# Kernel tuning notes

Measured on AMD Instinct MI355X. Metric: run time of the kernel, lower is better.

Reference implementation:

```python
import jax, jax.numpy as jnp
import numpy as np

K_DIM = 128

def setup_inputs() -> dict:
    key = jax.random.key(0)
    k1, k2, k3, k4 = jax.random.split(key, 4)
    B, S, D = 4, 4096, 1024
    input_vec = jax.random.normal(k1, (B, S, D), dtype=jnp.float32)
    # 'normal' Keras initializer ~ RandomNormal(stddev=0.05)
    weight_query = jax.random.normal(k2, (D, K_DIM), dtype=jnp.float32) * 0.05
    weight_key = jax.random.normal(k3, (D, K_DIM), dtype=jnp.float32) * 0.05
    weight_value = jax.random.normal(k4, (D, K_DIM), dtype=jnp.float32) * 0.05
    return {"input_vec": input_vec, "weight_query": weight_query,
            "weight_key": weight_key, "weight_value": weight_value}

def reference(input_vec, weight_query, weight_key, weight_value):
    # Q/K/V projections: [B,S,D] @ [D,K] -> [B,S,K]
    q = jnp.einsum('bsd,dk->bsk', input_vec, weight_query)
    k = jnp.einsum('bsd,dk->bsk', input_vec, weight_key)
    v = jnp.einsum('bsd,dk->bsk', input_vec, weight_value)
    scale = 1.0 / jnp.sqrt(jnp.asarray(K_DIM, dtype=q.dtype))
    # full score matrix [B,S,S], softmax over last axis (keys)
    scores = jnp.einsum('bqk,bsk->bqs', q, k) * scale
    attn = jax.nn.softmax(scores, axis=-1)
    return jnp.einsum('bqs,bsk->bqk', attn, v)
```

## Files before the change

### kernel.cpp

```cpp
#include <hip/hip_runtime.h>
#include <hip/hip_bf16.h>
#include <math.h>

#define B_  4
#define S_  4096
#define D_  1024
#define KD_ 128
#define NSPL 4
#define NIT64 (S_ / NSPL / 64)

typedef __attribute__((ext_vector_type(8))) short short8;
typedef __attribute__((ext_vector_type(4))) float f32x4;
typedef __attribute__((ext_vector_type(16))) float f32x16;
typedef __attribute__((ext_vector_type(4))) unsigned short us4;
typedef __attribute__((ext_vector_type(4))) unsigned int u32x4;

__device__ __forceinline__ unsigned short f2bf(float f) {
    __hip_bfloat16 h = __float2bfloat16(f);
    return *reinterpret_cast<unsigned short*>(&h);
}

__device__ __forceinline__ f32x4 mfma_bf16(short8 a, short8 b, f32x4 c) {
    return __builtin_amdgcn_mfma_f32_16x16x32_bf16(a, b, c, 0, 0, 0);
}

__device__ __forceinline__ f32x16 mfma32_bf16(short8 a, short8 b, f32x16 c) {
    return __builtin_amdgcn_mfma_f32_32x32x16_bf16(a, b, c, 0, 0, 0);
}

__device__ __forceinline__ unsigned int cvt_pk_bf16(float lo, float hi_) {
    unsigned int r;
    asm("v_cvt_pk_bf16_f32 %0, %1, %2" : "=v"(r) : "v"(lo), "v"(hi_));
    return r;
}

__device__ __forceinline__ void g2l16(const void* g, void* l) {
    __builtin_amdgcn_global_load_lds(
        (const __attribute__((address_space(1))) unsigned int*)g,
        (__attribute__((address_space(3))) unsigned int*)l, 16, 0, 0);
}

__global__ void convert_w_kernel(const float* __restrict__ wq,
                                 const float* __restrict__ wk,
                                 const float* __restrict__ wv,
                                 unsigned short* __restrict__ wt) {
    int t = blockIdx.x * 256 + threadIdx.x;
    int w = t >> 14;
    int r = t & 16383;
    int n = r & 127;
    int k8 = r >> 7;
    const float* src = (w == 0) ? wq : (w == 1) ? wk : wv;
    float scale = (w == 0) ? 0.12751725551033443f : 1.0f;
    short8 v;
#pragma unroll
    for (int i = 0; i < 8; ++i)
        v[i] = (short)f2bf(src[(size_t)(k8 * 8 + i) * KD_ + n] * scale);
    *reinterpret_cast<short8*>(&wt[(size_t)w * KD_ * D_ + (size_t)n * D_ + k8 * 8]) = v;
}

__global__ __launch_bounds__(512) void proj_kernel(
        const float* __restrict__ X, const unsigned short* __restrict__ Wt,
        unsigned short* __restrict__ Qo, unsigned short* __restrict__ Ko,
        unsigned short* __restrict__ Vt) {
    const int bid = blockIdx.x;
    const int g = bid / 24;
    const int local = bid - g * 24;
    const int which = local >> 3;
    const int mtile = g * 8 + (local & 7);
    const int m0 = mtile * 128;
    const int tid = threadIdx.x;
    const int lane = tid & 63;
    const int wid = tid >> 6;
    const int wr = wid >> 2, wc = wid & 3;
    const int l15 = lane & 15, l4 = lane >> 4;

    __shared__ __align__(16) unsigned short Asm[128 * 64];
    __shared__ __align__(16) unsigned short Bsm[128 * 64];
    __shared__ __align__(16) unsigned short Tsm[128 * 128];

    const unsigned short* W = Wt + (size_t)which * KD_ * D_;

    f32x4 acc[4][2];
#pragma unroll
    for (int r = 0; r < 4; ++r)
#pragma unroll
        for (int c = 0; c < 2; ++c) acc[r][c] = (f32x4)0.0f;

    for (int k0 = 0; k0 < D_; k0 += 64) {
#pragma unroll
        for (int i = 0; i < 4; ++i) {
            int f = tid + i * 512;
            int row = f >> 4, c4 = f & 15;
            float4 xv = *reinterpret_cast<const float4*>(
                &X[(size_t)(m0 + row) * D_ + k0 + c4 * 4]);
            us4 h;
            h.x = f2bf(xv.x); h.y = f2bf(xv.y); h.z = f2bf(xv.z); h.w = f2bf(xv.w);
            int gw = c4 >> 1, half = c4 & 1;
            *reinterpret_cast<us4*>(
                &Asm[row * 64 + ((gw ^ (row & 7)) * 8) + half * 4]) = h;
        }
#pragma unroll
        for (int i = 0; i < 2; ++i) {
            int gg = tid + i * 512;
            int n = gg >> 3, c8 = gg & 7;
            *reinterpret_cast<short8*>(&Bsm[n * 64 + ((c8 ^ (n & 7)) * 8)]) =
                *reinterpret_cast<const short8*>(&W[(size_t)n * D_ + k0 + c8 * 8]);
        }
        __syncthreads();

        short8 a[4][2], b[2][2];
#pragma unroll
        for (int rt = 0; rt < 4; ++rt)
#pragma unroll
            for (int kc = 0; kc < 2; ++kc) {
                int row = wr * 64 + rt * 16 + l15;
                int gr = kc * 4 + l4;
                a[rt][kc] = *reinterpret_cast<const short8*>(
                    &Asm[row * 64 + ((gr ^ (row & 7)) * 8)]);
            }
#pragma unroll
        for (int ct = 0; ct < 2; ++ct)
#pragma unroll
            for (int kc = 0; kc < 2; ++kc) {
                int row = wc * 32 + ct * 16 + l15;
                int gr = kc * 4 + l4;
                b[ct][kc] = *reinterpret_cast<const short8*>(
                    &Bsm[row * 64 + ((gr ^ (row & 7)) * 8)]);
            }
        __builtin_amdgcn_s_setprio(1);
#pragma unroll
        for (int kc = 0; kc < 2; ++kc)
#pragma unroll
            for (int rt = 0; rt < 4; ++rt)
#pragma unroll
                for (int ct = 0; ct < 2; ++ct)
                    acc[rt][ct] = mfma_bf16(a[rt][kc], b[ct][kc], acc[rt][ct]);
        __builtin_amdgcn_s_setprio(0);
        __syncthreads();
    }

    if (which < 2) {
        unsigned short* O = (which == 0) ? Qo : Ko;
#pragma unroll
        for (int rt = 0; rt < 4; ++rt)
#pragma unroll
            for (int ct = 0; ct < 2; ++ct)
#pragma unroll
                for (int j = 0; j < 4; ++j) {
                    int row = m0 + wr * 64 + rt * 16 + l4 * 4 + j;
                    int col = wc * 32 + ct * 16 + l15;
                    O[(size_t)row * KD_ + col] = f2bf(acc[rt][ct][j]);
                }
    } else {
#pragma unroll
        for (int rt = 0; rt < 4; ++rt)
#pragma unroll
            for (int ct = 0; ct < 2; ++ct)
#pragma unroll
                for (int j = 0; j < 4; ++j) {
                    int row = wr * 64 + rt * 16 + l4 * 4 + j;
                    int col = wc * 32 + ct * 16 + l15;
                    Tsm[col * 128 + row] = f2bf(acc[rt][ct][j]);
                }
        __syncthreads();
        int bb = m0 >> 12;
        int s0 = m0 & 4095;
#pragma unroll
        for (int i = 0; i < 4; ++i) {
            int gg = tid + i * 512;
            int n = gg >> 4, s8 = gg & 15;
            *reinterpret_cast<short8*>(
                &Vt[(size_t)bb * KD_ * S_ + (size_t)n * S_ + s0 + s8 * 8]) =
                *reinterpret_cast<short8*>(&Tsm[n * 128 + s8 * 8]);
        }
    }
}

__global__ __launch_bounds__(256, 2) void attn_split_kernel(
        const unsigned short* __restrict__ Q,
        const unsigned short* __restrict__ Kb,
        const unsigned short* __restrict__ Vt,
        unsigned short* __restrict__ part16, float* __restrict__ lsumP) {
    const int bid = blockIdx.x;
    const int b  = bid & 3;
    const int s  = (bid >> 2) & 3;
    const int qt = bid >> 4;
    const int tid = threadIdx.x;
    const int lane = tid & 63;
    const int wid = tid >> 6;
    const int q0 = qt * 128;
    const int l31 = lane & 31;
    const int hi  = lane >> 5;

    __shared__ __align__(16) unsigned short Ksm[2][64 * 128];
    __shared__ __align__(16) unsigned short Vsm[2][128 * 64];

    short8 aq[8];
    {
        const unsigned short* qrow =
            Q + ((size_t)(b * S_ + q0 + wid * 32 + l31)) * KD_;
#pragma unroll
        for (int kc = 0; kc < 8; ++kc)
            aq[kc] = *reinterpret_cast<const short8*>(&qrow[kc * 16 + hi * 8]);
    }

    f32x16 o[4];
#pragma unroll
    for (int dt = 0; dt < 4; ++dt) o[dt] = (f32x16)0.0f;
    float lsA = 0.0f, lsB = 0.0f;

    const unsigned short* Kbase = Kb + (size_t)b * S_ * KD_;
    const unsigned short* Vbase = Vt + (size_t)b * KD_ * S_;

    auto STAGE = [&](int buf, int kt) {
#pragma unroll
        for (int i = 0; i < 4; ++i) {
            int d = i * 256 + wid * 64 + lane;
            int row = d >> 4, c = d & 15;
            g2l16(&Kbase[(size_t)(kt * 64 + row) * KD_ + ((c ^ (row & 15)) * 8)],
                  &Ksm[buf][(i * 256 + wid * 64) * 8]);
        }
#pragma unroll
        for (int i = 0; i < 4; ++i) {
            int d = i * 256 + wid * 64 + lane;
            int row = d >> 3, c = d & 7;
            g2l16(&Vbase[(size_t)row * S_ + kt * 64 + ((c ^ (row & 7)) * 8)],
                  &Vsm[buf][(i * 256 + wid * 64) * 8]);
        }
    };

    const int base = s * NIT64;
    STAGE(0, base);

    for (int it = 0; it < NIT64; ++it) {
        asm volatile("s_waitcnt vmcnt(0)" ::: "memory");
        __builtin_amdgcn_s_barrier();
        if (it + 1 < NIT64) STAGE((it + 1) & 1, base + it + 1);

        const unsigned short* ksm = &Ksm[it & 1][0];
        const unsigned short* vsm = &Vsm[it & 1][0];

#pragma unroll
        for (int h = 0; h < 2; ++h) {
            f32x16 sf = (f32x16)0.0f;
            __builtin_amdgcn_s_setprio(1);
#pragma unroll
            for (int kc = 0; kc < 8; ++kc) {
                int row = h * 32 + l31;
                short8 bk = *reinterpret_cast<const short8*>(
                    &ksm[row * 128 + (((kc * 2 + hi) ^ (l31 & 15)) * 8)]);
                sf = mfma32_bf16(bk, aq[kc], sf);
            }
            __builtin_amdgcn_s_setprio(0);

            float p[16];
#pragma unroll
            for (int r = 0; r < 16; ++r) {
                p[r] = exp2f(sf[r]);
                if (r & 1) lsB += p[r]; else lsA += p[r];
            }

            short8 pa[2];
#pragma unroll
            for (int c = 0; c < 2; ++c) {
                u32x4 wv;
#pragma unroll
                for (int e = 0; e < 2; ++e) {
                    unsigned int X = cvt_pk_bf16(p[8 * c + 2 * e], p[8 * c + 2 * e + 1]);
                    unsigned int Y = cvt_pk_bf16(p[8 * c + 4 + 2 * e], p[8 * c + 4 + 2 * e + 1]);
                    unsigned int Ss = hi ? X : Y;
                    unsigned int T = __shfl_xor(Ss, 32);
                    wv[e]     = hi ? T : X;
                    wv[2 + e] = hi ? Y : T;
                }
                pa[c] = __builtin_bit_cast(short8, wv);
            }

            __builtin_amdgcn_s_setprio(1);
#pragma unroll
            for (int c = 0; c < 2; ++c)
#pragma unroll
                for (int dt = 0; dt < 4; ++dt) {
                    int row = dt * 32 + l31;
                    int gr = (h * 2 + c) * 2 + hi;
                    short8 bv = *reinterpret_cast<const short8*>(
                        &vsm[row * 64 + ((gr ^ (row & 7)) * 8)]);
                    o[dt] = mfma32_bf16(pa[c], bv, o[dt]);
                }
            __builtin_amdgcn_s_setprio(0);
        }
    }

    float lsum = lsA + lsB;
    lsum += __shfl_xor(lsum, 32);

    const int tile = (qt << 2) | b;
    unsigned short* Po = part16 + ((size_t)tile * NSPL + s) * 16384;
#pragma unroll
    for (int r = 0; r < 16; ++r) {
        int row = wid * 32 + (r & 3) + 8 * (r >> 2) + 4 * hi;
#pragma unroll
        for (int dt = 0; dt < 4; ++dt)
            Po[row * 128 + dt * 32 + l31] = f2bf(o[dt][r]);
    }
    if (hi == 0)
        lsumP[((size_t)tile * NSPL + s) * 128 + wid * 32 + l31] = lsum;
}

__global__ __launch_bounds__(256) void merge_kernel(
        const unsigned short* __restrict__ part16,
        const float* __restrict__ lsumP, float* __restrict__ Out) {
    const int th = blockIdx.x;
    const int tile = th >> 1;
    const int half = th & 1;
    const int b = tile & 3, qt = tile >> 2;
    const int r0 = half * 64;
    const int tid = threadIdx.x;
    __shared__ float inv[64];
    if (tid < 64) {
        const float* lp = lsumP + (size_t)tile * (NSPL * 128) + r0;
        float t = 0.0f;
#pragma unroll
        for (int s = 0; s < NSPL; ++s) t += lp[s * 128 + tid];
        inv[tid] = 1.0f / t;
    }
    __syncthreads();
    const unsigned short* p = part16 + (size_t)tile * NSPL * 16384 + r0 * 128;
    float* Ob = Out + ((size_t)b * S_ + qt * 128 + r0) * KD_;
#pragma unroll
    for (int i = 0; i < 4; ++i) {
        int g = tid + i * 256;
        int row = g >> 4;
        float acc8[8] = {0, 0, 0, 0, 0, 0, 0, 0};
#pragma unroll
        for (int s = 0; s < NSPL; ++s) {
            short8 v = *reinterpret_cast<const short8*>(&p[s * 16384 + g * 8]);
#pragma unroll
            for (int j = 0; j < 8; ++j) {
                unsigned int u = ((unsigned int)(unsigned short)v[j]) << 16;
                acc8[j] += __uint_as_float(u);
            }
        }
        float iv = inv[row];
        float4 r0v, r1v;
        r0v.x = acc8[0] * iv; r0v.y = acc8[1] * iv;
        r0v.z = acc8[2] * iv; r0v.w = acc8[3] * iv;
        r1v.x = acc8[4] * iv; r1v.y = acc8[5] * iv;
        r1v.z = acc8[6] * iv; r1v.w = acc8[7] * iv;
        *reinterpret_cast<float4*>(&Ob[g * 8]) = r0v;
        *reinterpret_cast<float4*>(&Ob[g * 8 + 4]) = r1v;
    }
}

__global__ __launch_bounds__(512, 2) void attn_kernel(
        const unsigned short* __restrict__ Q,
        const unsigned short* __restrict__ Kb,
        const unsigned short* __restrict__ Vt,
        float* __restrict__ Out) {
    const int bid = blockIdx.x;
    const int b  = bid & 3;
    const int qt = bid >> 2;
    const int tid = threadIdx.x;
    const int lane = tid & 63;
    const int wid = tid >> 6;
    const int grp = wid >> 1;
    const int wg  = wid & 1;
    const int q0 = qt * 64;
    const int l31 = lane & 31;
    const int hi  = lane >> 5;

    __shared__ __align__(16) unsigned char lds_raw[131072];
    unsigned short* KsmA = (unsigned short*)lds_raw;
    unsigned short* VsmA = (unsigned short*)(lds_raw + 65536);

    short8 aq[8];
    {
        const unsigned short* qrow =
            Q + ((size_t)(b * S_ + q0 + wg * 32 + l31)) * KD_;
#pragma unroll
        for (int kc = 0; kc < 8; ++kc)
            aq[kc] = *reinterpret_cast<const short8*>(&qrow[kc * 16 + hi * 8]);
    }

    f32x16 o[4];
#pragma unroll
    for (int dt = 0; dt < 4; ++dt) o[dt] = (f32x16)0.0f;
    float lsum = 0.0f;

    const unsigned short* Kbase = Kb + (size_t)b * S_ * KD_;
    const unsigned short* Vbase = Vt + (size_t)b * KD_ * S_;

    unsigned short* Kgrp = KsmA + grp * 2 * 4096;
    unsigned short* Vgrp = VsmA + grp * 2 * 4096;

    auto STAGE = [&](int buf, int kt) {
#pragma unroll
        for (int i = 0; i < 4; ++i) {
            int d = i * 128 + wg * 64 + lane;
            int row = d >> 4, c = d & 15;
            g2l16(&Kbase[(size_t)(kt * 32 + row) * KD_ + ((c ^ (row & 15)) * 8)],
                  &Kgrp[(buf * 512 + i * 128 + wg * 64) * 8]);
        }
#pragma unroll
        for (int i = 0; i < 4; ++i) {
            int d = i * 128 + wg * 64 + lane;
            int row = d >> 2, c = d & 3;
            g2l16(&Vbase[(size_t)row * S_ + kt * 32 + ((c ^ ((row >> 1) & 3)) * 8)],
                  &Vgrp[(buf * 512 + i * 128 + wg * 64) * 8]);
        }
    };

    int cur = 0;
    STAGE(0, grp);
    __syncthreads();

    for (int it = 0; it < 32; ++it) {
        if (it < 31) STAGE(cur ^ 1, (it + 1) * 4 + grp);

        const unsigned short* ksm = Kgrp + cur * 4096;
        const unsigned short* vsm = Vgrp + cur * 4096;

        f32x16 sf = (f32x16)0.0f;
        __builtin_amdgcn_s_setprio(1);
#pragma unroll
        for (int kc = 0; kc < 8; ++kc) {
            short8 bk = *reinterpret_cast<const short8*>(
                &ksm[l31 * 128 + (((kc * 2 + hi) ^ (l31 & 15)) * 8)]);
            sf = mfma32_bf16(bk, aq[kc], sf);
        }
        __builtin_amdgcn_s_setprio(0);

        float p[16];
#pragma unroll
        for (int r = 0; r < 16; ++r) {
            p[r] = exp2f(sf[r]);
            lsum += p[r];
        }

        short8 pa[2];
#pragma unroll
        for (int c = 0; c < 2; ++c) {
            u32x4 wv;
#pragma unroll
            for (int e = 0; e < 2; ++e) {
                unsigned int X = cvt_pk_bf16(p[8 * c + 2 * e], p[8 * c + 2 * e + 1]);
                unsigned int Y = cvt_pk_bf16(p[8 * c + 4 + 2 * e], p[8 * c + 4 + 2 * e + 1]);
                unsigned int Ss = hi ? X : Y;
                unsigned int T = __shfl_xor(Ss, 32);
                wv[e]     = hi ? T : X;
                wv[2 + e] = hi ? Y : T;
            }
            pa[c] = __builtin_bit_cast(short8, wv);
        }

        __builtin_amdgcn_s_setprio(1);
#pragma unroll
        for (int c = 0; c < 2; ++c)
#pragma unroll
            for (int dt = 0; dt < 4; ++dt) {
                int row = dt * 32 + l31;
                short8 bv = *reinterpret_cast<const short8*>(
                    &vsm[row * 32 + (((c * 2 + hi) ^ ((row >> 1) & 3)) * 8)]);
                o[dt] = mfma32_bf16(pa[c], bv, o[dt]);
            }
        __builtin_amdgcn_s_setprio(0);

        __syncthreads();
        cur ^= 1;
    }

    lsum += __shfl_xor(lsum, 32);

    float* scratch = (float*)lds_raw;
    float* lsumS   = (float*)(lds_raw + 98304);
    __syncthreads();
    if (grp >= 1) {
        int base = (grp - 1) * 8192;
#pragma unroll
        for (int dt = 0; dt < 4; ++dt)
#pragma unroll
            for (int r = 0; r < 16; ++r) {
                int row = wg * 32 + (r & 3) + 8 * (r >> 2) + 4 * hi;
                scratch[base + row * 128 + dt * 32 + l31] = o[dt][r];
            }
    }
    if (hi == 0) lsumS[grp * 64 + wg * 32 + l31] = lsum;
    __syncthreads();
    if (grp == 0) {
        float* Ob = Out + (size_t)b * S_ * KD_;
#pragma unroll
        for (int r = 0; r < 16; ++r) {
            int row = wg * 32 + (r & 3) + 8 * (r >> 2) + 4 * hi;
            float inv = 1.0f / (lsumS[row] + lsumS[64 + row] +
                                lsumS[128 + row] + lsumS[192 + row]);
#pragma unroll
            for (int dt = 0; dt < 4; ++dt) {
                int col = dt * 32 + l31;
                int idx = row * 128 + col;
                float v = o[dt][r] + scratch[idx] + scratch[8192 + idx] +
                          scratch[16384 + idx];
                Ob[(size_t)(q0 + row) * KD_ + col] = v * inv;
            }
        }
    }
}

extern "C" void kernel_launch(void* const* d_in, const int* in_sizes, int n_in,
                              void* d_out, int out_size, void* d_ws, size_t ws_size,
                              hipStream_t stream) {
    const float* X  = (const float*)d_in[0];
    const float* Wq = (const float*)d_in[1];
    const float* Wk = (const float*)d_in[2];
    const float* Wv = (const float*)d_in[3];
    float* Out = (float*)d_out;

    unsigned short* Wt  = (unsigned short*)d_ws;
    unsigned short* Q16 = (unsigned short*)((char*)d_ws + 786432);
    unsigned short* K16 = Q16 + (size_t)16384 * 128;
    unsigned short* V16 = K16 + (size_t)16384 * 128;
    unsigned short* part16 = (unsigned short*)((char*)d_ws + 13369344);
    float* lsumP = (float*)((char*)d_ws + 13369344 + 16777216);
    const size_t ws_need = 13369344 + 16777216 + 262144;

    hipLaunchKernelGGL(convert_w_kernel, dim3(192), dim3(256), 0, stream,
                       Wq, Wk, Wv, Wt);
    hipLaunchKernelGGL(proj_kernel, dim3(384), dim3(512), 0, stream,
                       X, Wt, Q16, K16, V16);
    if (ws_size >= ws_need) {
        hipLaunchKernelGGL(attn_split_kernel, dim3(512), dim3(256), 0, stream,
                           Q16, K16, V16, part16, lsumP);
        hipLaunchKernelGGL(merge_kernel, dim3(256), dim3(256), 0, stream,
                           part16, lsumP, Out);
    } else {
        hipLaunchKernelGGL(attn_kernel, dim3(256), dim3(512), 0, stream,
                           Q16, K16, V16, Out);
    }
}
```

Measured before the change: 92.87 us.

## Double query rows per warp and raise key split count to eight

Each warp now handles 64 query rows (two 32-row MFMA tiles) instead of 32, so every K and V fragment read from LDS feeds two MFMAs. This raises operand reuse and halves LDS traffic per FLOP. To keep the grid at 512 blocks, the key dimension is split 8 ways instead of 4. The cost is higher register pressure (double accumulators and Q fragments under 2-blocks-per-SM launch bounds), plus twice the partial-output workspace and merge traffic.

```diff
diff --git a/kernel.cpp b/kernel.cpp
--- a/kernel.cpp
+++ b/kernel.cpp
@@ -6,8 +6,8 @@
 #define S_  4096
 #define D_  1024
 #define KD_ 128
-#define NSPL 4
-#define NIT64 (S_ / NSPL / 64)
+#define NSPL 8
+#define NIT8 (S_ / NSPL / 64)
 
 typedef __attribute__((ext_vector_type(8))) short short8;
 typedef __attribute__((ext_vector_type(4))) float f32x4;
@@ -183,31 +183,34 @@
         unsigned short* __restrict__ part16, float* __restrict__ lsumP) {
     const int bid = blockIdx.x;
     const int b  = bid & 3;
-    const int s  = (bid >> 2) & 3;
-    const int qt = bid >> 4;
+    const int s  = (bid >> 2) & 7;
+    const int qt = bid >> 5;
     const int tid = threadIdx.x;
     const int lane = tid & 63;
     const int wid = tid >> 6;
-    const int q0 = qt * 128;
+    const int q0 = qt * 256;
     const int l31 = lane & 31;
     const int hi  = lane >> 5;
 
     __shared__ __align__(16) unsigned short Ksm[2][64 * 128];
     __shared__ __align__(16) unsigned short Vsm[2][128 * 64];
 
-    short8 aq[8];
-    {
+    short8 aq[2][8];
+#pragma unroll
+    for (int a = 0; a < 2; ++a) {
         const unsigned short* qrow =
-            Q + ((size_t)(b * S_ + q0 + wid * 32 + l31)) * KD_;
+            Q + ((size_t)(b * S_ + q0 + wid * 64 + a * 32 + l31)) * KD_;
 #pragma unroll
         for (int kc = 0; kc < 8; ++kc)
-            aq[kc] = *reinterpret_cast<const short8*>(&qrow[kc * 16 + hi * 8]);
-    }
-
-    f32x16 o[4];
-#pragma unroll
-    for (int dt = 0; dt < 4; ++dt) o[dt] = (f32x16)0.0f;
-    float lsA = 0.0f, lsB = 0.0f;
+            aq[a][kc] = *reinterpret_cast<const short8*>(&qrow[kc * 16 + hi * 8]);
+    }
+
+    f32x16 o[2][4];
+#pragma unroll
+    for (int a = 0; a < 2; ++a)
+#pragma unroll
+        for (int dt = 0; dt < 4; ++dt) o[a][dt] = (f32x16)0.0f;
+    float ls[2] = {0.0f, 0.0f};
 
     const unsigned short* Kbase = Kb + (size_t)b * S_ * KD_;
     const unsigned short* Vbase = Vt + (size_t)b * KD_ * S_;
@@ -229,51 +232,55 @@
         }
     };
 
-    const int base = s * NIT64;
+    const int base = s * NIT8;
     STAGE(0, base);
 
-    for (int it = 0; it < NIT64; ++it) {
+    for (int it = 0; it < NIT8; ++it) {
         asm volatile("s_waitcnt vmcnt(0)" ::: "memory");
         __builtin_amdgcn_s_barrier();
-        if (it + 1 < NIT64) STAGE((it + 1) & 1, base + it + 1);
+        if (it + 1 < NIT8) STAGE((it + 1) & 1, base + it + 1);
 
         const unsigned short* ksm = &Ksm[it & 1][0];
         const unsigned short* vsm = &Vsm[it & 1][0];
 
 #pragma unroll
         for (int h = 0; h < 2; ++h) {
-            f32x16 sf = (f32x16)0.0f;
+            f32x16 sf[2];
+            sf[0] = (f32x16)0.0f; sf[1] = (f32x16)0.0f;
             __builtin_amdgcn_s_setprio(1);
 #pragma unroll
             for (int kc = 0; kc < 8; ++kc) {
                 int row = h * 32 + l31;
                 short8 bk = *reinterpret_cast<const short8*>(
                     &ksm[row * 128 + (((kc * 2 + hi) ^ (l31 & 15)) * 8)]);
-                sf = mfma32_bf16(bk, aq[kc], sf);
+                sf[0] = mfma32_bf16(bk, aq[0][kc], sf[0]);
+                sf[1] = mfma32_bf16(bk, aq[1][kc], sf[1]);
             }
             __builtin_amdgcn_s_setprio(0);
 
-            float p[16];
-#pragma unroll
-            for (int r = 0; r < 16; ++r) {
-                p[r] = exp2f(sf[r]);
-                if (r & 1) lsB += p[r]; else lsA += p[r];
-            }
-
-            short8 pa[2];
-#pragma unroll
-            for (int c = 0; c < 2; ++c) {
-                u32x4 wv;
-#pragma unroll
-                for (int e = 0; e < 2; ++e) {
-                    unsigned int X = cvt_pk_bf16(p[8 * c + 2 * e], p[8 * c + 2 * e + 1]);
-                    unsigned int Y = cvt_pk_bf16(p[8 * c + 4 + 2 * e], p[8 * c + 4 + 2 * e + 1]);
-                    unsigned int Ss = hi ? X : Y;
-                    unsigned int T = __shfl_xor(Ss, 32);
-                    wv[e]     = hi ? T : X;
-                    wv[2 + e] = hi ? Y : T;
+            short8 pa[2][2];
+#pragma unroll
+            for (int a = 0; a < 2; ++a) {
+                float p[16];
+#pragma unroll
+                for (int r = 0; r < 16; ++r) {
+                    p[r] = exp2f(sf[a][r]);
+                    ls[a] += p[r];
                 }
-                pa[c] = __builtin_bit_cast(short8, wv);
+#pragma unroll
+                for (int c = 0; c < 2; ++c) {
+                    u32x4 wv;
+#pragma unroll
+                    for (int e = 0; e < 2; ++e) {
+                        unsigned int X = cvt_pk_bf16(p[8 * c + 2 * e], p[8 * c + 2 * e + 1]);
+                        unsigned int Y = cvt_pk_bf16(p[8 * c + 4 + 2 * e], p[8 * c + 4 + 2 * e + 1]);
+                        unsigned int Ss = hi ? X : Y;
+                        unsigned int T = __shfl_xor(Ss, 32);
+                        wv[e]     = hi ? T : X;
+                        wv[2 + e] = hi ? Y : T;
+                    }
+                    pa[a][c] = __builtin_bit_cast(short8, wv);
+                }
             }
 
             __builtin_amdgcn_s_setprio(1);
@@ -285,48 +292,55 @@
                     int gr = (h * 2 + c) * 2 + hi;
                     short8 bv = *reinterpret_cast<const short8*>(
                         &vsm[row * 64 + ((gr ^ (row & 7)) * 8)]);
-                    o[dt] = mfma32_bf16(pa[c], bv, o[dt]);
+                    o[0][dt] = mfma32_bf16(pa[0][c], bv, o[0][dt]);
+                    o[1][dt] = mfma32_bf16(pa[1][c], bv, o[1][dt]);
                 }
             __builtin_amdgcn_s_setprio(0);
         }
     }
 
-    float lsum = lsA + lsB;
-    lsum += __shfl_xor(lsum, 32);
+#pragma unroll
+    for (int a = 0; a < 2; ++a)
+        ls[a] += __shfl_xor(ls[a], 32);
 
     const int tile = (qt << 2) | b;
-    unsigned short* Po = part16 + ((size_t)tile * NSPL + s) * 16384;
-#pragma unroll
-    for (int r = 0; r < 16; ++r) {
-        int row = wid * 32 + (r & 3) + 8 * (r >> 2) + 4 * hi;
-#pragma unroll
-        for (int dt = 0; dt < 4; ++dt)
-            Po[row * 128 + dt * 32 + l31] = f2bf(o[dt][r]);
-    }
-    if (hi == 0)
-        lsumP[((size_t)tile * NSPL + s) * 128 + wid * 32 + l31] = lsum;
+    unsigned short* Po = part16 + ((size_t)tile * NSPL + s) * 32768;
+#pragma unroll
+    for (int a = 0; a < 2; ++a)
+#pragma unroll
+        for (int r = 0; r < 16; ++r) {
+            int row = wid * 64 + a * 32 + (r & 3) + 8 * (r >> 2) + 4 * hi;
+#pragma unroll
+            for (int dt = 0; dt < 4; ++dt)
+                Po[row * 128 + dt * 32 + l31] = f2bf(o[a][dt][r]);
+        }
+    if (hi == 0) {
+#pragma unroll
+        for (int a = 0; a < 2; ++a)
+            lsumP[((size_t)tile * NSPL + s) * 256 + wid * 64 + a * 32 + l31] = ls[a];
+    }
 }
 
 __global__ __launch_bounds__(256) void merge_kernel(
         const unsigned short* __restrict__ part16,
         const float* __restrict__ lsumP, float* __restrict__ Out) {
     const int th = blockIdx.x;
-    const int tile = th >> 1;
-    const int half = th & 1;
+    const int tile = th >> 2;
+    const int quarter = th & 3;
     const int b = tile & 3, qt = tile >> 2;
-    const int r0 = half * 64;
+    const int r0 = quarter * 64;
     const int tid = threadIdx.x;
     __shared__ float inv[64];
     if (tid < 64) {
-        const float* lp = lsumP + (size_t)tile * (NSPL * 128) + r0;
+        const float* lp = lsumP + (size_t)tile * (NSPL * 256) + r0;
         float t = 0.0f;
 #pragma unroll
-        for (int s = 0; s < NSPL; ++s) t += lp[s * 128 + tid];
+        for (int s = 0; s < NSPL; ++s) t += lp[s * 256 + tid];
         inv[tid] = 1.0f / t;
     }
     __syncthreads();
-    const unsigned short* p = part16 + (size_t)tile * NSPL * 16384 + r0 * 128;
-    float* Ob = Out + ((size_t)b * S_ + qt * 128 + r0) * KD_;
+    const unsigned short* p = part16 + (size_t)tile * NSPL * 32768 + r0 * 128;
+    float* Ob = Out + ((size_t)b * S_ + qt * 256 + r0) * KD_;
 #pragma unroll
     for (int i = 0; i < 4; ++i) {
         int g = tid + i * 256;
@@ -334,7 +348,7 @@
         float acc8[8] = {0, 0, 0, 0, 0, 0, 0, 0};
 #pragma unroll
         for (int s = 0; s < NSPL; ++s) {
-            short8 v = *reinterpret_cast<const short8*>(&p[s * 16384 + g * 8]);
+            short8 v = *reinterpret_cast<const short8*>(&p[s * 32768 + g * 8]);
 #pragma unroll
             for (int j = 0; j < 8; ++j) {
                 unsigned int u = ((unsigned int)(unsigned short)v[j]) << 16;
@@ -519,8 +533,8 @@
     unsigned short* K16 = Q16 + (size_t)16384 * 128;
     unsigned short* V16 = K16 + (size_t)16384 * 128;
     unsigned short* part16 = (unsigned short*)((char*)d_ws + 13369344);
-    float* lsumP = (float*)((char*)d_ws + 13369344 + 16777216);
-    const size_t ws_need = 13369344 + 16777216 + 262144;
+    float* lsumP = (float*)((char*)d_ws + 13369344 + 33554432);
+    const size_t ws_need = 13369344 + 33554432 + 524288;
 
     hipLaunchKernelGGL(convert_w_kernel, dim3(192), dim3(256), 0, stream,
                        Wq, Wk, Wv, Wt);
```

New measurement: 143.6 us. 1.55x slower.
